# Optimization experiments

Hardware: AMD Instinct MI355X
Metric: run time of the kernel (lower is better)

The kernel has to match this reference:

```python
import jax, jax.numpy as jnp
import numpy as np

D_MODEL = 1024
H = 16
D_K = D_MODEL // H
D_FF = 4096
EPS = 1e-6


def setup_inputs() -> dict:
    key = jax.random.key(0)
    ks = jax.random.split(key, 12)
    B, S = 8, 1024
    s = 0.02
    inp = {
        "x": jax.random.normal(ks[0], (B, S, D_MODEL), dtype=jnp.float32),
        "src_mask": jnp.ones((B, 1, 1, S), dtype=jnp.int32),
        "wq": jax.random.normal(ks[1], (D_MODEL, D_MODEL), dtype=jnp.float32) * s,
        "bq": jnp.zeros((D_MODEL,), jnp.float32),
        "wk": jax.random.normal(ks[2], (D_MODEL, D_MODEL), dtype=jnp.float32) * s,
        "bk": jnp.zeros((D_MODEL,), jnp.float32),
        "wv": jax.random.normal(ks[3], (D_MODEL, D_MODEL), dtype=jnp.float32) * s,
        "bv": jnp.zeros((D_MODEL,), jnp.float32),
        "wo": jax.random.normal(ks[4], (D_MODEL, D_MODEL), dtype=jnp.float32) * s,
        "bo": jnp.zeros((D_MODEL,), jnp.float32),
        "w1": jax.random.normal(ks[5], (D_FF, D_MODEL), dtype=jnp.float32) * s,
        "b1": jnp.zeros((D_FF,), jnp.float32),
        "w2": jax.random.normal(ks[6], (D_MODEL, D_FF), dtype=jnp.float32) * s,
        "b2": jnp.zeros((D_MODEL,), jnp.float32),
        "ln1_a": jnp.ones((1,), jnp.float32),
        "ln1_b": jnp.zeros((1,), jnp.float32),
        "ln2_a": jnp.ones((1,), jnp.float32),
        "ln2_b": jnp.zeros((1,), jnp.float32),
    }
    return inp


def _layernorm(x, alpha, bias):
    # matches torch: std with Bessel correction (ddof=1), eps added to std
    mean = jnp.mean(x, axis=-1, keepdims=True)
    std = jnp.std(x, axis=-1, keepdims=True, ddof=1)
    return (x - mean) / (std + EPS) * alpha + bias


def reference(x, src_mask, wq, bq, wk, bk, wv, bv, wo, bo, w1, b1, w2, b2,
              ln1_a, ln1_b, ln2_a, ln2_b):
    B, S, _ = x.shape
    # --- residual 1: self attention on pre-normed x ---
    n = _layernorm(x, ln1_a, ln1_b)
    q = n @ wq.T + bq
    # NOTE: the source has a bug: key and value are views of the *query*
    # projection (w_k/w_v outputs are computed but discarded). We reproduce it.
    _ = n @ wk.T + bk
    _ = n @ wv.T + bv
    qh = q.reshape(B, S, H, D_K).transpose(0, 2, 1, 3)  # [B,H,S,dk]
    kh = qh
    vh = qh
    scores = jnp.einsum('bhqd,bhkd->bhqk', qh, kh) / jnp.sqrt(jnp.float32(D_K))
    scores = jnp.where(src_mask == 0, jnp.float32(-1e9), scores)
    attn = jax.nn.softmax(scores, axis=-1)
    ctx = jnp.einsum('bhqk,bhkd->bhqd', attn, vh)
    ctx = ctx.transpose(0, 2, 1, 3).reshape(B, S, D_MODEL)
    x = x + (ctx @ wo.T + bo)
    # --- residual 2: feed-forward (intended ReLU MLP) ---
    n2 = _layernorm(x, ln2_a, ln2_b)
    h = jax.nn.relu(n2 @ w1.T + b1)
    x = x + (h @ w2.T + b2)
    return x
```

## Files before the change

### kernel.cpp

```cpp
#include <hip/hip_runtime.h>
#include <hip/hip_bf16.h>

typedef __attribute__((ext_vector_type(8))) short short8;
typedef __attribute__((ext_vector_type(4))) float f32x4;

#define MFMA16(a, b, c) __builtin_amdgcn_mfma_f32_16x16x32_bf16((a), (b), (c), 0, 0, 0)

__device__ __forceinline__ unsigned short f2bf(float f) {
  union { float f; unsigned int u; } v; v.f = f;
  return (unsigned short)((v.u + 0x7fffu + ((v.u >> 16) & 1u)) >> 16);
}

__device__ __forceinline__ void gload_lds16(const void* g, void* l) {
  __builtin_amdgcn_global_load_lds((__attribute__((address_space(1))) void*)g,
                                   (__attribute__((address_space(3))) void*)l,
                                   16, 0, 0);
}

struct CvtArgs {
  const float* s0; const float* s1; const float* s2; const float* s3;
  unsigned short* d0; unsigned short* d1; unsigned short* d2; unsigned short* d3;
};

__global__ __launch_bounds__(256) void cvt_weights(CvtArgs a) {
  const long N0 = 1048576, N1 = 1048576, N2 = 4194304;
  long i = ((long)blockIdx.x * 256 + threadIdx.x) * 4;
  const float* s; unsigned short* d; long off;
  if (i < N0)                { s = a.s0; d = a.d0; off = i; }
  else if (i < N0 + N1)      { s = a.s1; d = a.d1; off = i - N0; }
  else if (i < N0 + N1 + N2) { s = a.s2; d = a.d2; off = i - N0 - N1; }
  else                       { s = a.s3; d = a.d3; off = i - N0 - N1 - N2; }
  float4 v = *(const float4*)(s + off);
  ushort4 o;
  o.x = f2bf(v.x); o.y = f2bf(v.y); o.z = f2bf(v.z); o.w = f2bf(v.w);
  *(ushort4*)(d + off) = o;
}

__global__ __launch_bounds__(256) void ln_kernel(
    const float* __restrict__ x,
    const float* __restrict__ alpha, const float* __restrict__ beta,
    unsigned short* __restrict__ out) {
  const int row = blockIdx.x;
  const int tid = threadIdx.x;
  const float4 v = ((const float4*)(x + (size_t)row * 1024))[tid];
  float s  = v.x + v.y + v.z + v.w;
  float sq = v.x * v.x + v.y * v.y + v.z * v.z + v.w * v.w;
  #pragma unroll
  for (int d = 32; d >= 1; d >>= 1) {
    s  += __shfl_xor(s, d, 64);
    sq += __shfl_xor(sq, d, 64);
  }
  __shared__ float red[8];
  const int w = tid >> 6;
  if ((tid & 63) == 0) { red[w] = s; red[4 + w] = sq; }
  __syncthreads();
  s  = red[0] + red[1] + red[2] + red[3];
  sq = red[4] + red[5] + red[6] + red[7];
  const float mean = s * (1.f / 1024.f);
  float var = (sq - s * mean) * (1.f / 1023.f);
  var = fmaxf(var, 0.f);
  const float rs = alpha[0] / (sqrtf(var) + 1e-6f);
  const float bb = beta[0];
  ushort4 o;
  o.x = f2bf((v.x - mean) * rs + bb);
  o.y = f2bf((v.y - mean) * rs + bb);
  o.z = f2bf((v.z - mean) * rs + bb);
  o.w = f2bf((v.w - mean) * rs + bb);
  ((ushort4*)out)[(size_t)row * 256 + tid] = o;
}

template <int OUT_BF16, int RELU, int NF>
__global__ __launch_bounds__(512, 2) void gemm2ph(
    const unsigned short* __restrict__ A, int lda,
    const unsigned short* __restrict__ B, int ldb,
    const float* __restrict__ bias,
    const float* __restrict__ residual,
    void* __restrict__ Cout,
    int M, int N, int K, float cscale, int nbx) {
  __shared__ __align__(16) unsigned short lds[32768 + NF * 8192];
  const int NT = K >> 6;
  const int tid = threadIdx.x;
  const int w = tid >> 6, lane = tid & 63;
  const int cpx = gridDim.x >> 3;
  const int id = (blockIdx.x & 7) * cpx + (blockIdx.x >> 3);
  const int bx = id % nbx, by = id / nbx;
  const int row0 = by * 256, col0 = bx * (NF * 64);
  const int wr128 = (w >> 2) * 128, wcN = (w & 3) * (NF * 16);
  const int lq = lane & 15, g = lane >> 4, g4 = g * 4;
  const int strow = tid >> 3;
  const int sunit8 = ((tid & 7) ^ (strow & 7)) * 8;

  const unsigned short* Asrc = A + (size_t)(row0 + strow) * lda + sunit8;
  const unsigned short* Bsrc = B + (size_t)(col0 + strow) * ldb + sunit8;

  auto stage = [&](int buf, int tt) {
    unsigned short* Ad = lds + buf * 16384 + w * 512;
    unsigned short* Bd = lds + 32768 + buf * (NF * 4096) + w * 512;
    #pragma unroll
    for (int c = 0; c < 4; ++c)
      gload_lds16(Asrc + (size_t)(c * 64) * lda + tt * 64, Ad + c * 4096);
    #pragma unroll
    for (int c = 0; c < NF; ++c)
      gload_lds16(Bsrc + (size_t)(c * 64) * ldb + tt * 64, Bd + c * 4096);
  };

  f32x4 acc[8][NF] = {};

  stage(0, 0);
  asm volatile("s_waitcnt vmcnt(0)" ::: "memory");
  __builtin_amdgcn_s_barrier();
  int buf = 0;

  for (int t = 0; t < NT; ++t) {
    if (t + 1 < NT) stage(buf ^ 1, t + 1);
    const unsigned short* Ab = lds + buf * 16384;
    const unsigned short* Bb = lds + 32768 + buf * (NF * 4096);
    #pragma unroll
    for (int kk = 0; kk < 2; ++kk) {
      short8 af[8], bf[NF];
      #pragma unroll
      for (int m = 0; m < 8; ++m) {
        const int r = wr128 + m * 16 + lq;
        af[m] = *(const short8*)(Ab + r * 64 + (((kk * 4 + g) ^ (r & 7)) << 3));
      }
      #pragma unroll
      for (int n = 0; n < NF; ++n) {
        const int r = wcN + n * 16 + lq;
        bf[n] = *(const short8*)(Bb + r * 64 + (((kk * 4 + g) ^ (r & 7)) << 3));
      }
      __builtin_amdgcn_s_setprio(1);
      #pragma unroll
      for (int m = 0; m < 8; ++m)
        #pragma unroll
        for (int n = 0; n < NF; ++n)
          acc[m][n] = MFMA16(af[m], bf[n], acc[m][n]);
      __builtin_amdgcn_s_setprio(0);
    }
    if (t + 1 < NT) {
      asm volatile("s_waitcnt vmcnt(0)" ::: "memory");
      __builtin_amdgcn_s_barrier();
      buf ^= 1;
    }
  }

  float bv[NF];
  #pragma unroll
  for (int n = 0; n < NF; ++n) bv[n] = bias[col0 + wcN + n * 16 + lq];

  if (OUT_BF16) {
    const int CW = NF * 64 + 4;
    unsigned short* cbuf = lds;
    __syncthreads();
    #pragma unroll
    for (int p = 0; p < 2; ++p) {
      if ((w >> 2) == p) {
        #pragma unroll
        for (int m = 0; m < 8; ++m)
          #pragma unroll
          for (int n = 0; n < NF; ++n)
            #pragma unroll
            for (int r = 0; r < 4; ++r) {
              float v = (acc[m][n][r] + bv[n]) * cscale;
              if (RELU) v = fmaxf(v, 0.f);
              cbuf[(m * 16 + g4 + r) * CW + wcN + n * 16 + lq] = f2bf(v);
            }
      }
      __syncthreads();
      #pragma unroll
      for (int i = 0; i < 2 * NF; ++i) {
        const int un = i * 512 + tid;
        const int row = un / (8 * NF);
        const int cu = un % (8 * NF);
        const short8 vv = *(const short8*)&cbuf[row * CW + cu * 8];
        *(short8*)((unsigned short*)Cout + (size_t)(row0 + p * 128 + row) * N + col0 + cu * 8) = vv;
      }
      __syncthreads();
    }
  } else {
    #pragma unroll
    for (int n = 0; n < NF; ++n) {
      const int col = col0 + wcN + n * 16 + lq;
      #pragma unroll
      for (int m = 0; m < 8; ++m) {
        #pragma unroll
        for (int r = 0; r < 4; ++r) {
          const int row = row0 + wr128 + m * 16 + g4 + r;
          float v = (acc[m][n][r] + bv[n]) * cscale;
          if (RELU) v = fmaxf(v, 0.f);
          const size_t idx = (size_t)row * N + col;
          if (residual) v += residual[idx];
          ((float*)Cout)[idx] = v;
        }
      }
    }
  }
}

__global__ __launch_bounds__(256) void transpose_q(
    const unsigned short* __restrict__ q, unsigned short* __restrict__ qT) {
  const int st = blockIdx.x, bh = blockIdx.y;
  const int b = bh >> 4, h = bh & 15;
  __shared__ __align__(16) unsigned short tile[64][80];
  const int tid = threadIdx.x;
  const unsigned short* src = q + ((size_t)(b * 1024 + st * 64)) * 1024 + h * 64;
  #pragma unroll
  for (int j = 0; j < 2; ++j) {
    const int u = tid + j * 256;
    const int sl = u >> 3, d8 = (u & 7) * 8;
    *(short8*)&tile[sl][d8] = *(const short8*)&src[(size_t)sl * 1024 + d8];
  }
  __syncthreads();
  unsigned short* dst = qT + ((size_t)(bh * 64)) * 1024 + st * 64;
  #pragma unroll
  for (int j = 0; j < 2; ++j) {
    const int u = tid + j * 256;
    const int dl = u >> 3, s8 = (u & 7) * 8;
    short8 o;
    #pragma unroll
    for (int i = 0; i < 8; ++i) o[i] = (short)tile[s8 + i][dl];
    *(short8*)&dst[(size_t)dl * 1024 + s8] = o;
  }
}

__global__ __launch_bounds__(256) void attn_kernel(
    const unsigned short* __restrict__ q,
    const unsigned short* __restrict__ qT,
    const int* __restrict__ mask,
    unsigned short* __restrict__ ctx) {
  __shared__ __align__(16) unsigned short Ks[2][64 * 64];
  __shared__ __align__(16) unsigned short Vs[2][64 * 64];
  __shared__ int allmask;
  const int id = blockIdx.x;
  const int bh = ((id & 7) << 4) + (id >> 6);
  const int qt = (id >> 3) & 7;
  const int b = bh >> 4, h = bh & 15;
  const int tid = threadIdx.x, w = tid >> 6, lane = tid & 63;
  const int lq = lane & 15;
  const int g = lane >> 4;
  const int lk8 = g * 8;
  const int swz = lane & 7;
  const int q0 = qt * 128 + w * 32;
  const size_t qbase = (size_t)b * (1024 * 1024) + h * 64;
  const size_t qTb = (size_t)bh * 64 * 1024;
  const int srow = lane >> 3;
  const int su = (lane & 7) ^ srow;
  const size_t ksrc = qbase + (size_t)(w * 16 + srow) * 1024 + su * 8;
  const size_t vsrc = qTb + (size_t)(w * 16 + srow) * 1024 + su * 8;
  const float RS = 2.3548202f;

  auto stage = [&](int bufi, int kt) {
    char* Kd = (char*)Ks[bufi] + w * 2048;
    char* Vd = (char*)Vs[bufi] + w * 2048;
    gload_lds16(q + ksrc + (size_t)(kt * 64) * 1024, Kd);
    gload_lds16(q + ksrc + (size_t)(kt * 64 + 8) * 1024, Kd + 1024);
    gload_lds16(qT + vsrc + kt * 64, Vd);
    gload_lds16(qT + vsrc + (size_t)8 * 1024 + kt * 64, Vd + 1024);
  };

  const int* mrow = mask + b * 1024;
  if (tid == 0) allmask = 1;
  int mp = 1;
  #pragma unroll
  for (int i = 0; i < 4; ++i) mp &= (mrow[tid + i * 256] != 0);
  stage(0, 0);
  __syncthreads();
  if (!__all(mp) && lane == 0) atomicAnd(&allmask, 0);
  asm volatile("s_waitcnt vmcnt(0)" ::: "memory");
  __syncthreads();
  const bool fullmask = (allmask != 0);

  short8 qa[2][2];
  #pragma unroll
  for (int qf = 0; qf < 2; ++qf)
    #pragma unroll
    for (int kk = 0; kk < 2; ++kk)
      qa[qf][kk] = *(const short8*)&q[qbase + (size_t)(q0 + qf * 16 + lq) * 1024 + kk * 32 + lk8];

  short8 ones;
  #pragma unroll
  for (int i = 0; i < 8; ++i) ones[i] = (short)0x3F80;

  f32x4 lacc[2] = {};
  f32x4 Oa[2][4];
  #pragma unroll
  for (int mf = 0; mf < 2; ++mf)
    #pragma unroll
    for (int nf = 0; nf < 4; ++nf) Oa[mf][nf] = (f32x4){0.f, 0.f, 0.f, 0.f};

  int cur = 0;

  for (int kt = 0; kt < 16; ++kt) {
    const int k0 = kt * 64;
    if (kt < 15) stage(cur ^ 1, kt + 1);
    const char* Kb = (const char*)Ks[cur];
    const char* Vb = (const char*)Vs[cur];
    f32x4 s[2][4];
    #pragma unroll
    for (int qf = 0; qf < 2; ++qf)
      #pragma unroll
      for (int kf = 0; kf < 4; ++kf) s[qf][kf] = (f32x4){0.f, 0.f, 0.f, 0.f};
    #pragma unroll
    for (int kf = 0; kf < 4; ++kf) {
      const char* kr = Kb + (kf * 16 + lq) * 128;
      const short8 ka0 = *(const short8*)(kr + (((g) ^ swz) << 4));
      const short8 ka1 = *(const short8*)(kr + (((4 + g) ^ swz) << 4));
      s[0][kf] = MFMA16(ka0, qa[0][0], s[0][kf]);
      s[0][kf] = MFMA16(ka1, qa[0][1], s[0][kf]);
      s[1][kf] = MFMA16(ka0, qa[1][0], s[1][kf]);
      s[1][kf] = MFMA16(ka1, qa[1][1], s[1][kf]);
    }
    if (!fullmask) {
      #pragma unroll
      for (int kf = 0; kf < 4; ++kf) {
        const int4 mv = *(const int4*)&mrow[k0 + kf * 16 + g * 4];
        float madd[4];
        madd[0] = mv.x ? 0.f : -1e9f; madd[1] = mv.y ? 0.f : -1e9f;
        madd[2] = mv.z ? 0.f : -1e9f; madd[3] = mv.w ? 0.f : -1e9f;
        #pragma unroll
        for (int qf = 0; qf < 2; ++qf)
          #pragma unroll
          for (int r = 0; r < 4; ++r)
            s[qf][kf][r] += madd[r];
      }
    }
    unsigned int E[2][4], O[2][4];
    #pragma unroll
    for (int qf = 0; qf < 2; ++qf) {
      #pragma unroll
      for (int kf = 0; kf < 4; ++kf) {
        float p0 = exp2f(s[qf][kf][0]);
        float p1 = exp2f(s[qf][kf][1]);
        float p2 = exp2f(s[qf][kf][2]);
        float p3 = exp2f(s[qf][kf][3]);
        asm("v_cvt_pk_bf16_f32 %0, %1, %2" : "=v"(E[qf][kf]) : "v"(p0), "v"(p1));
        asm("v_cvt_pk_bf16_f32 %0, %1, %2" : "=v"(O[qf][kf]) : "v"(p2), "v"(p3));
      }
    }
    short8 pa[2][2];
    #pragma unroll
    for (int qf = 0; qf < 2; ++qf) {
      #pragma unroll
      for (int ks = 0; ks < 2; ++ks) {
        unsigned int e0 = E[qf][2 * ks], e1 = E[qf][2 * ks + 1];
        unsigned int o0 = O[qf][2 * ks], o1 = O[qf][2 * ks + 1];
        asm("v_permlane32_swap_b32 %0, %1" : "+v"(e0), "+v"(e1));
        asm("v_permlane16_swap_b32 %0, %1" : "+v"(e0), "+v"(e1));
        asm("v_permlane32_swap_b32 %0, %1" : "+v"(o0), "+v"(o1));
        asm("v_permlane16_swap_b32 %0, %1" : "+v"(o0), "+v"(o1));
        union { unsigned int u[4]; short8 s8; } pw;
        pw.u[0] = e0; pw.u[1] = o0; pw.u[2] = e1; pw.u[3] = o1;
        pa[qf][ks] = pw.s8;
      }
    }
    #pragma unroll
    for (int ks = 0; ks < 2; ++ks) {
      #pragma unroll
      for (int nf = 0; nf < 4; ++nf) {
        const short8 vb = *(const short8*)(Vb + (nf * 16 + lq) * 128 + (((4 * ks + g) ^ swz) << 4));
        Oa[0][nf] = MFMA16(pa[0][ks], vb, Oa[0][nf]);
        Oa[1][nf] = MFMA16(pa[1][ks], vb, Oa[1][nf]);
      }
      lacc[0] = MFMA16(pa[0][ks], ones, lacc[0]);
      lacc[1] = MFMA16(pa[1][ks], ones, lacc[1]);
    }
    __syncthreads();
    cur ^= 1;
  }
  #pragma unroll
  for (int mf = 0; mf < 2; ++mf) {
    #pragma unroll
    for (int r = 0; r < 4; ++r) {
      const float linv = RS / lacc[mf][r];
      const int row = q0 + mf * 16 + g * 4 + r;
      #pragma unroll
      for (int nf = 0; nf < 4; ++nf) {
        const int col = h * 64 + nf * 16 + lq;
        ctx[((size_t)b * 1024 + row) * 1024 + col] = f2bf(Oa[mf][nf][r] * linv);
      }
    }
  }
}

extern "C" void kernel_launch(void* const* d_in, const int* in_sizes, int n_in,
                              void* d_out, int out_size, void* d_ws, size_t ws_size,
                              hipStream_t stream) {
  const float* x    = (const float*)d_in[0];
  const int*   mask = (const int*)d_in[1];
  const float* wq   = (const float*)d_in[2];
  const float* bq   = (const float*)d_in[3];
  const float* wo   = (const float*)d_in[8];
  const float* bo   = (const float*)d_in[9];
  const float* w1   = (const float*)d_in[10];
  const float* b1   = (const float*)d_in[11];
  const float* w2   = (const float*)d_in[12];
  const float* b2   = (const float*)d_in[13];
  const float* ln1a = (const float*)d_in[14];
  const float* ln1b = (const float*)d_in[15];
  const float* ln2a = (const float*)d_in[16];
  const float* ln2b = (const float*)d_in[17];
  float* out = (float*)d_out;

  char* ws = (char*)d_ws;
  unsigned short* wq_b  = (unsigned short*)(ws);
  unsigned short* wo_b  = (unsigned short*)(ws + (2l << 20));
  unsigned short* w1_b  = (unsigned short*)(ws + (4l << 20));
  unsigned short* w2_b  = (unsigned short*)(ws + (12l << 20));
  unsigned short* n_b   = (unsigned short*)(ws + (20l << 20));
  unsigned short* q_b   = (unsigned short*)(ws + (36l << 20));
  unsigned short* qT_b  = (unsigned short*)(ws + (52l << 20));
  unsigned short* ctx_b = (unsigned short*)(ws + (68l << 20));
  unsigned short* h_b   = (unsigned short*)(ws + (84l << 20));

  const float SQRT_SC = 0.42466090f;

  CvtArgs ca{wq, wo, w1, w2, wq_b, wo_b, w1_b, w2_b};
  cvt_weights<<<10240, 256, 0, stream>>>(ca);
  ln_kernel<<<8192, 256, 0, stream>>>(x, ln1a, ln1b, n_b);
  gemm2ph<1, 0, 2><<<256, 512, 0, stream>>>(n_b, 1024, wq_b, 1024, bq, nullptr, q_b, 8192, 1024, 1024, SQRT_SC, 8);
  transpose_q<<<dim3(16, 128), 256, 0, stream>>>(q_b, qT_b);
  attn_kernel<<<1024, 256, 0, stream>>>(q_b, qT_b, mask, ctx_b);
  gemm2ph<0, 0, 2><<<256, 512, 0, stream>>>(ctx_b, 1024, wo_b, 1024, bo, x, out, 8192, 1024, 1024, 1.0f, 8);
  ln_kernel<<<8192, 256, 0, stream>>>(out, ln2a, ln2b, n_b);
  gemm2ph<1, 1, 4><<<512, 512, 0, stream>>>(n_b, 1024, w1_b, 1024, b1, nullptr, h_b, 8192, 4096, 1024, 1.0f, 16);
  gemm2ph<0, 0, 2><<<256, 512, 0, stream>>>(h_b, 4096, w2_b, 4096, b2, out, out, 8192, 1024, 4096, 1.0f, 8);
}
```

Baseline: 316.7 us.

## Fuse Q transpose into Q-projection epilogue and stage fp32 epilogue through LDS

```diff
diff --git a/kernel.cpp b/kernel.cpp
--- a/kernel.cpp
+++ b/kernel.cpp
@@ -69,13 +69,14 @@
   ((ushort4*)out)[(size_t)row * 256 + tid] = o;
 }
 
-template <int OUT_BF16, int RELU, int NF>
+template <int OUT_BF16, int RELU, int NF, int WQT>
 __global__ __launch_bounds__(512, 2) void gemm2ph(
     const unsigned short* __restrict__ A, int lda,
     const unsigned short* __restrict__ B, int ldb,
     const float* __restrict__ bias,
     const float* __restrict__ residual,
     void* __restrict__ Cout,
+    unsigned short* __restrict__ qTout,
     int M, int N, int K, float cscale, int nbx) {
   __shared__ __align__(16) unsigned short lds[32768 + NF * 8192];
   const int NT = K >> 6;
@@ -174,51 +175,60 @@
         const short8 vv = *(const short8*)&cbuf[row * CW + cu * 8];
         *(short8*)((unsigned short*)Cout + (size_t)(row0 + p * 128 + row) * N + col0 + cu * 8) = vv;
       }
+      if (WQT) {
+        const int grow = row0 + p * 128;
+        const int bb = grow >> 10;
+        const int s0 = grow & 1023;
+        const int h0 = col0 >> 6;
+        #pragma unroll
+        for (int i = 0; i < 4; ++i) {
+          const int un = i * 512 + tid;
+          const int colx = un >> 4;
+          const int su = un & 15;
+          const int hh = h0 + (colx >> 6);
+          const int dd = colx & 63;
+          short8 o;
+          #pragma unroll
+          for (int j = 0; j < 8; ++j) o[j] = (short)cbuf[(su * 8 + j) * CW + colx];
+          *(short8*)(qTout + ((size_t)(bb * 16 + hh) * 64 + dd) * 1024 + s0 + su * 8) = o;
+        }
+      }
       __syncthreads();
     }
   } else {
-    #pragma unroll
-    for (int n = 0; n < NF; ++n) {
-      const int col = col0 + wcN + n * 16 + lq;
-      #pragma unroll
-      for (int m = 0; m < 8; ++m) {
+    const int CWf = NF * 64 + 4;
+    float* cbuf = (float*)lds;
+    __syncthreads();
+    #pragma unroll
+    for (int p = 0; p < 2; ++p) {
+      if ((w >> 2) == p) {
         #pragma unroll
-        for (int r = 0; r < 4; ++r) {
-          const int row = row0 + wr128 + m * 16 + g4 + r;
-          float v = (acc[m][n][r] + bv[n]) * cscale;
-          if (RELU) v = fmaxf(v, 0.f);
-          const size_t idx = (size_t)row * N + col;
-          if (residual) v += residual[idx];
-          ((float*)Cout)[idx] = v;
+        for (int m = 0; m < 8; ++m)
+          #pragma unroll
+          for (int n = 0; n < NF; ++n)
+            #pragma unroll
+            for (int r = 0; r < 4; ++r) {
+              float v = (acc[m][n][r] + bv[n]) * cscale;
+              if (RELU) v = fmaxf(v, 0.f);
+              cbuf[(m * 16 + g4 + r) * CWf + wcN + n * 16 + lq] = v;
+            }
+      }
+      __syncthreads();
+      #pragma unroll
+      for (int i = 0; i < 4 * NF; ++i) {
+        const int un = i * 512 + tid;
+        const int row = un / (16 * NF);
+        const int cu = un % (16 * NF);
+        float4 v = *(const float4*)&cbuf[row * CWf + cu * 4];
+        const size_t idx = (size_t)(row0 + p * 128 + row) * N + col0 + cu * 4;
+        if (residual) {
+          const float4 rv = *(const float4*)(residual + idx);
+          v.x += rv.x; v.y += rv.y; v.z += rv.z; v.w += rv.w;
         }
-      }
-    }
-  }
-}
-
-__global__ __launch_bounds__(256) void transpose_q(
-    const unsigned short* __restrict__ q, unsigned short* __restrict__ qT) {
-  const int st = blockIdx.x, bh = blockIdx.y;
-  const int b = bh >> 4, h = bh & 15;
-  __shared__ __align__(16) unsigned short tile[64][80];
-  const int tid = threadIdx.x;
-  const unsigned short* src = q + ((size_t)(b * 1024 + st * 64)) * 1024 + h * 64;
-  #pragma unroll
-  for (int j = 0; j < 2; ++j) {
-    const int u = tid + j * 256;
-    const int sl = u >> 3, d8 = (u & 7) * 8;
-    *(short8*)&tile[sl][d8] = *(const short8*)&src[(size_t)sl * 1024 + d8];
-  }
-  __syncthreads();
-  unsigned short* dst = qT + ((size_t)(bh * 64)) * 1024 + st * 64;
-  #pragma unroll
-  for (int j = 0; j < 2; ++j) {
-    const int u = tid + j * 256;
-    const int dl = u >> 3, s8 = (u & 7) * 8;
-    short8 o;
-    #pragma unroll
-    for (int i = 0; i < 8; ++i) o[i] = (short)tile[s8 + i][dl];
-    *(short8*)&dst[(size_t)dl * 1024 + s8] = o;
+        *(float4*)((float*)Cout + idx) = v;
+      }
+      __syncthreads();
+    }
   }
 }
 
@@ -416,11 +426,10 @@
   CvtArgs ca{wq, wo, w1, w2, wq_b, wo_b, w1_b, w2_b};
   cvt_weights<<<10240, 256, 0, stream>>>(ca);
   ln_kernel<<<8192, 256, 0, stream>>>(x, ln1a, ln1b, n_b);
-  gemm2ph<1, 0, 2><<<256, 512, 0, stream>>>(n_b, 1024, wq_b, 1024, bq, nullptr, q_b, 8192, 1024, 1024, SQRT_SC, 8);
-  transpose_q<<<dim3(16, 128), 256, 0, stream>>>(q_b, qT_b);
+  gemm2ph<1, 0, 2, 1><<<256, 512, 0, stream>>>(n_b, 1024, wq_b, 1024, bq, nullptr, q_b, qT_b, 8192, 1024, 1024, SQRT_SC, 8);
   attn_kernel<<<1024, 256, 0, stream>>>(q_b, qT_b, mask, ctx_b);
-  gemm2ph<0, 0, 2><<<256, 512, 0, stream>>>(ctx_b, 1024, wo_b, 1024, bo, x, out, 8192, 1024, 1024, 1.0f, 8);
+  gemm2ph<0, 0, 2, 0><<<256, 512, 0, stream>>>(ctx_b, 1024, wo_b, 1024, bo, x, out, nullptr, 8192, 1024, 1024, 1.0f, 8);
   ln_kernel<<<8192, 256, 0, stream>>>(out, ln2a, ln2b, n_b);
-  gemm2ph<1, 1, 4><<<512, 512, 0, stream>>>(n_b, 1024, w1_b, 1024, b1, nullptr, h_b, 8192, 4096, 1024, 1.0f, 16);
-  gemm2ph<0, 0, 2><<<256, 512, 0, stream>>>(h_b, 4096, w2_b, 4096, b2, out, out, 8192, 1024, 4096, 1.0f, 8);
-}
+  gemm2ph<1, 1, 4, 0><<<512, 512, 0, stream>>>(n_b, 1024, w1_b, 1024, b1, nullptr, h_b, nullptr, 8192, 4096, 1024, 1.0f, 16);
+  gemm2ph<0, 0, 2, 0><<<256, 512, 0, stream>>>(h_b, 4096, w2_b, 4096, b2, out, out, nullptr, 8192, 1024, 4096, 1.0f, 8);
+}
```

Measured after the change: 296.5 us. -6.4%, faster.
